# Kernel optimization log

Measured on AMD Instinct MI355X. Metric: run time of the kernel, lower is better.

Reference implementation:

```python
import jax, jax.numpy as jnp
from jax import lax
import numpy as np

HID = 64
NL = 4

def conv2d(x, w, b):
    # x: (N,C,H,W), w: (O,I,kh,kw)
    y = lax.conv_general_dilated(x, w, (1, 1), 'SAME',
                                 dimension_numbers=('NCHW', 'OIHW', 'NCHW'))
    return y + b[None, :, None, None]


def stlstm_cell(x, h, c, m, Wx, bx, Wh, bh, Wm, bm, Wo, bo, Wl, bl):
    # standard PredRNN SpatioTemporalLSTM cell
    xc = conv2d(x, Wx, bx)            # 7*HID channels
    hc = conv2d(h, Wh, bh)            # 4*HID
    mc = conv2d(m, Wm, bm)            # 3*HID
    ix, fx, gx, ixp, fxp, gxp, ox = jnp.split(xc, 7, axis=1)
    ih, fh, gh, oh = jnp.split(hc, 4, axis=1)
    im, fm, gm = jnp.split(mc, 3, axis=1)
    i_t = jax.nn.sigmoid(ix + ih)
    f_t = jax.nn.sigmoid(fx + fh)
    g_t = jnp.tanh(gx + gh)
    c_new = f_t * c + i_t * g_t
    i_tp = jax.nn.sigmoid(ixp + im)
    f_tp = jax.nn.sigmoid(fxp + fm)
    g_tp = jnp.tanh(gxp + gm)
    m_new = f_tp * m + i_tp * g_tp
    mem = jnp.concatenate([c_new, m_new], axis=1)  # 2*HID
    o_t = jax.nn.sigmoid(ox + oh + conv2d(mem, Wo, bo))
    h_new = o_t * jnp.tanh(conv2d(mem, Wl, bl))
    return h_new, c_new, m_new


def setup_inputs() -> dict:
    key = jax.random.key(0)
    ks = jax.random.split(key, 16)
    B, L, C, H, W = 8, 10, 1, 256, 256
    x = jax.random.normal(ks[0], (B, L, C, H, W), dtype=jnp.float32)
    s = 0.02
    d = dict(
        x=x, in_len=10, out_len=10,
        Wx=jax.random.normal(ks[1], (NL, 7 * HID, HID, 3, 3), jnp.float32) * s,
        bx=jnp.zeros((NL, 7 * HID), jnp.float32),
        Wh=jax.random.normal(ks[2], (NL, 4 * HID, HID, 3, 3), jnp.float32) * s,
        bh=jnp.zeros((NL, 4 * HID), jnp.float32),
        Wm=jax.random.normal(ks[3], (NL, 3 * HID, HID, 3, 3), jnp.float32) * s,
        bm=jnp.zeros((NL, 3 * HID), jnp.float32),
        Wo=jax.random.normal(ks[4], (NL, HID, 2 * HID, 3, 3), jnp.float32) * s,
        bo=jnp.zeros((NL, HID), jnp.float32),
        Wl=jax.random.normal(ks[5], (NL, HID, 2 * HID, 1, 1), jnp.float32) * s,
        bl=jnp.zeros((NL, HID), jnp.float32),
        Wd=jax.random.normal(ks[6], (64, HID, 3, 3), jnp.float32) * s,
        bd=jnp.zeros((64,), jnp.float32),
    )
    return d


def reference(x, in_len, out_len, Wx, bx, Wh, bh, Wm, bm, Wo, bo, Wl, bl, Wd, bd):
    B, L, C, H, W = x.shape
    ph, pw = H // 8, W // 8
    # patch_division: space-to-depth 8x8
    xp = x.reshape(B, L, C, 8, ph, 8, pw).transpose(0, 1, 2, 3, 5, 4, 6)
    xp = xp.reshape(B, L, C * 64, ph, pw)
    T = in_len + out_len - 1  # 19 steps
    pad = jnp.zeros((B, T - in_len, C * 64, ph, pw), xp.dtype)
    xs_seq = jnp.moveaxis(jnp.concatenate([xp, pad], axis=1), 1, 0)  # (T,B,64,ph,pw)
    flags = jnp.arange(T) < in_len
    z = jnp.zeros((NL, B, HID, ph, pw), xp.dtype)
    carry0 = (z, z, jnp.zeros((B, HID, ph, pw), xp.dtype),
              jnp.zeros((B, HID, ph, pw), xp.dtype))

    def step(carry, inp):
        hs, cs, m, htop = carry
        xt, flag = inp
        cur = jnp.where(flag, xt, htop)
        new_h, new_c = [], []
        for l in range(NL):
            h, c, m = stlstm_cell(cur, hs[l], cs[l], m,
                                  Wx[l], bx[l], Wh[l], bh[l], Wm[l], bm[l],
                                  Wo[l], bo[l], Wl[l], bl[l])
            new_h.append(h)
            new_c.append(c)
            cur = h
        return (jnp.stack(new_h), jnp.stack(new_c), m, cur), cur

    _, outs = lax.scan(step, carry0, (xs_seq, flags))  # (T,B,HID,ph,pw)
    y = jnp.moveaxis(outs, 0, 1).reshape(B * T, HID, ph, pw)
    y = jax.nn.sigmoid(conv2d(y, Wd, bd)).reshape(B, T, 64, ph, pw)
    # patch_combination: depth-to-space 8x8
    out = y.reshape(B, T, 1, 8, 8, ph, pw).transpose(0, 1, 2, 3, 5, 4, 6)
    out = out.reshape(B, T, 1, 8 * ph, 8 * pw)
    return out
```

## Files before the change

kernel.cpp:

```cpp
#include <hip/hip_runtime.h>
#include <hip/hip_bf16.h>


typedef __bf16 bf16x8 __attribute__((ext_vector_type(8)));
typedef float f32x4 __attribute__((ext_vector_type(4)));

namespace {
constexpr int  T     = 19;
constexpr int  INLEN = 10;

constexpr long OFF_XPB   = 0;
constexpr long OFF_OUTSB = 2621440;
constexpr long OFF_HB    = 7602176;
constexpr long OFF_MB    = 8650752;
constexpr long OFF_C     = 9175040;
constexpr long OFF_M     = 11272192;
constexpr long OFF_MEMB  = 11796480;
constexpr long OFF_OP    = 12320768;
constexpr long OFF_WFA   = 12845056;
constexpr long OFF_WFB   = 13877248;
constexpr long OFF_WFD   = 14041088;
constexpr long OFF_BA    = 14059520;
constexpr long WS_NEEDED_FLOATS = 14061312;
}

__device__ __forceinline__ float sigf(float x)     { return 1.f / (1.f + __expf(-x)); }
__device__ __forceinline__ float tanhfast(float x) { return 2.f / (1.f + __expf(-2.f * x)) - 1.f; }
__device__ __forceinline__ unsigned short f2b(float f) {
  __hip_bfloat16 h = __float2bfloat16(f);
  return __builtin_bit_cast(unsigned short, h);
}
__device__ __forceinline__ f32x4 mfma16(bf16x8 a, bf16x8 b, f32x4 c) {
  return __builtin_amdgcn_mfma_f32_16x16x32_bf16(a, b, c, 0, 0, 0);
}

__global__ __launch_bounds__(448) void kcellA(
    const unsigned short* __restrict__ in0, long in0bs,
    const unsigned short* __restrict__ hB,
    const unsigned short* __restrict__ mBr,
    const unsigned short* __restrict__ wfA,
    const float* __restrict__ bA,
    float* __restrict__ C, float* __restrict__ M,
    unsigned short* __restrict__ mBw,
    unsigned short* __restrict__ memB,
    float* __restrict__ op)
{
  __shared__ __align__(16) char smem[57344];
  unsigned short* sIn = (unsigned short*)smem;
  float* sEx = (float*)smem;

  const int b = blockIdx.x, r0 = blockIdx.y, tid = threadIdx.x;
  const unsigned short* base0 = in0 + (long)b * in0bs;
  const unsigned short* base1 = hB  + (long)b * 65536;
  const unsigned short* base2 = mBr + (long)b * 65536;

  for (int s = tid; s < 3 * 816; s += 448) {
    int inp = s / 816, rem = s - inp * 816;
    int slot = rem >> 3, cg = rem & 7;
    int rr = slot / 34, cl = slot - rr * 34;
    int gr = r0 - 1 + rr, gc = cl - 1;
    const unsigned short* bp = (inp == 0) ? base0 : ((inp == 1) ? base1 : base2);
    uint4 v = make_uint4(0u, 0u, 0u, 0u);
    if ((unsigned)gr < 32u && (unsigned)gc < 32u)
      v = *(const uint4*)(bp + ((long)(gr * 32 + gc) << 6) + cg * 8);
    *(uint4*)(sIn + inp * 6528 + slot * 64 + ((cg ^ (slot & 7)) * 8)) = v;
  }
  __syncthreads();

  const int w = tid >> 6, lane = tid & 63, q = lane >> 4, n16 = lane & 15;
  f32x4 acc[4][2];
  #pragma unroll
  for (int i = 0; i < 4; ++i) { acc[i][0] = (f32x4){0,0,0,0}; acc[i][1] = (f32x4){0,0,0,0}; }

  const unsigned short* sb1 = sIn + ((w < 4) ? 6528 : 13056);
  const unsigned short* wbase = wfA + (long)w * 73728;

  #pragma unroll
  for (int p = 0; p < 2; ++p) {
    const unsigned short* sb = p ? sb1 : sIn;
    #pragma unroll
    for (int tap = 0; tap < 9; ++tap) {
      const int dy = tap / 3, dx = tap - dy * 3;
      #pragma unroll
      for (int cc = 0; cc < 2; ++cc) {
        const unsigned short* wp = wbase + (long)(((p * 9 + tap) * 2 + cc) * 4) * 512 + lane * 8;
        bf16x8 a0 = *(const bf16x8*)(wp);
        bf16x8 a1 = *(const bf16x8*)(wp + 512);
        bf16x8 a2 = *(const bf16x8*)(wp + 1024);
        bf16x8 a3 = *(const bf16x8*)(wp + 1536);
        const int g = cc * 4 + q;
        bf16x8 bf0, bf1;
        { int slot = dy * 34 + n16 + dx;
          bf0 = *(const bf16x8*)(sb + slot * 64 + ((g ^ (slot & 7)) * 8)); }
        { int slot = dy * 34 + 16 + n16 + dx;
          bf1 = *(const bf16x8*)(sb + slot * 64 + ((g ^ (slot & 7)) * 8)); }
        acc[0][0] = mfma16(a0, bf0, acc[0][0]); acc[0][1] = mfma16(a0, bf1, acc[0][1]);
        acc[1][0] = mfma16(a1, bf0, acc[1][0]); acc[1][1] = mfma16(a1, bf1, acc[1][1]);
        acc[2][0] = mfma16(a2, bf0, acc[2][0]); acc[2][1] = mfma16(a2, bf1, acc[2][1]);
        acc[3][0] = mfma16(a3, bf0, acc[3][0]); acc[3][1] = mfma16(a3, bf1, acc[3][1]);
      }
    }
  }

  __syncthreads();
  #pragma unroll
  for (int i = 0; i < 4; ++i)
    #pragma unroll
    for (int j = 0; j < 2; ++j)
      #pragma unroll
      for (int r = 0; r < 4; ++r)
        sEx[w * 2048 + (i * 16 + q * 4 + r) * 32 + (j * 16 + n16)] = acc[i][j][r];
  __syncthreads();

  for (int idx = tid; idx < 2048; idx += 448) {
    const int ch = idx >> 5, pxl = idx & 31;
    const int pxg = r0 * 32 + pxl;
    float iv = sEx[idx]            + bA[ch];
    float fv = sEx[2048 + idx]     + bA[64 + ch];
    float gv = sEx[4096 + idx]     + bA[128 + ch];
    float ov = sEx[6144 + idx]     + bA[192 + ch];
    float i2 = sEx[8192 + idx]     + bA[256 + ch];
    float f2 = sEx[10240 + idx]    + bA[320 + ch];
    float g2 = sEx[12288 + idx]    + bA[384 + ch];
    const long cmo = ((long)b * 64 + ch) * 1024 + pxg;
    float cn = sigf(fv) * C[cmo] + sigf(iv) * tanhfast(gv);
    float mn = sigf(f2) * M[cmo] + sigf(i2) * tanhfast(g2);
    C[cmo] = cn; M[cmo] = mn; op[cmo] = ov;
    const long mo = (long)b * 1024 + pxg;
    memB[mo * 128 + ch]      = f2b(cn);
    memB[mo * 128 + 64 + ch] = f2b(mn);
    mBw[mo * 64 + ch]        = f2b(mn);
  }
}

__global__ __launch_bounds__(512) void kcellB(
    const unsigned short* __restrict__ memB,
    const unsigned short* __restrict__ wfB,
    const float* __restrict__ op, const float* __restrict__ bl,
    unsigned short* __restrict__ hBw, unsigned short* __restrict__ outsBt,
    int writeOuts)
{
  __shared__ __align__(16) char smem[73728];
  unsigned short* sIn = (unsigned short*)smem;
  float* sEx = (float*)smem;

  const int b = blockIdx.x, r0 = blockIdx.y, tid = threadIdx.x;
  const unsigned short* bp = memB + (long)b * 131072;
  for (int s = tid; s < 102 * 16; s += 512) {
    int slot = s >> 4, cg = s & 15;
    int rr = slot / 34, cl = slot - rr * 34;
    int gr = r0 - 1 + rr, gc = cl - 1;
    uint4 v = make_uint4(0u, 0u, 0u, 0u);
    if ((unsigned)gr < 32u && (unsigned)gc < 32u)
      v = *(const uint4*)(bp + ((long)(gr * 32 + gc) << 7) + cg * 8);
    *(uint4*)(sIn + slot * 128 + ((cg ^ (slot & 7)) * 8)) = v;
  }
  __syncthreads();

  const int w = tid >> 6, lane = tid & 63, q = lane >> 4, n16 = lane & 15;
  f32x4 accO[4][2], accL[4][2];
  #pragma unroll
  for (int i = 0; i < 4; ++i) {
    accO[i][0] = (f32x4){0,0,0,0}; accO[i][1] = (f32x4){0,0,0,0};
    accL[i][0] = (f32x4){0,0,0,0}; accL[i][1] = (f32x4){0,0,0,0};
  }

  #pragma unroll
  for (int s5 = 0; s5 < 5; ++s5) {
    const int s = w * 5 + s5;
    const bool isL = (s >= 36);
    const int tap = isL ? 4 : (s >> 2);
    const int cc  = isL ? (s - 36) : (s & 3);
    const int dy = tap / 3, dx = tap - dy * 3;
    const unsigned short* wp = wfB + (long)s * 2048 + lane * 8;
    bf16x8 a0 = *(const bf16x8*)(wp);
    bf16x8 a1 = *(const bf16x8*)(wp + 512);
    bf16x8 a2 = *(const bf16x8*)(wp + 1024);
    bf16x8 a3 = *(const bf16x8*)(wp + 1536);
    const int g = cc * 4 + q;
    bf16x8 bf0, bf1;
    { int slot = dy * 34 + n16 + dx;
      bf0 = *(const bf16x8*)(sIn + slot * 128 + ((g ^ (slot & 7)) * 8)); }
    { int slot = dy * 34 + 16 + n16 + dx;
      bf1 = *(const bf16x8*)(sIn + slot * 128 + ((g ^ (slot & 7)) * 8)); }
    if (isL) {
      accL[0][0] = mfma16(a0, bf0, accL[0][0]); accL[0][1] = mfma16(a0, bf1, accL[0][1]);
      accL[1][0] = mfma16(a1, bf0, accL[1][0]); accL[1][1] = mfma16(a1, bf1, accL[1][1]);
      accL[2][0] = mfma16(a2, bf0, accL[2][0]); accL[2][1] = mfma16(a2, bf1, accL[2][1]);
      accL[3][0] = mfma16(a3, bf0, accL[3][0]); accL[3][1] = mfma16(a3, bf1, accL[3][1]);
    } else {
      accO[0][0] = mfma16(a0, bf0, accO[0][0]); accO[0][1] = mfma16(a0, bf1, accO[0][1]);
      accO[1][0] = mfma16(a1, bf0, accO[1][0]); accO[1][1] = mfma16(a1, bf1, accO[1][1]);
      accO[2][0] = mfma16(a2, bf0, accO[2][0]); accO[2][1] = mfma16(a2, bf1, accO[2][1]);
      accO[3][0] = mfma16(a3, bf0, accO[3][0]); accO[3][1] = mfma16(a3, bf1, accO[3][1]);
    }
  }

  __syncthreads();
  #pragma unroll
  for (int i = 0; i < 4; ++i)
    #pragma unroll
    for (int j = 0; j < 2; ++j)
      #pragma unroll
      for (int r = 0; r < 4; ++r)
        sEx[w * 2048 + (i * 16 + q * 4 + r) * 32 + (j * 16 + n16)] = accO[i][j][r];
  if (w == 7) {
    #pragma unroll
    for (int i = 0; i < 4; ++i)
      #pragma unroll
      for (int j = 0; j < 2; ++j)
        #pragma unroll
        for (int r = 0; r < 4; ++r)
          sEx[16384 + (i * 16 + q * 4 + r) * 32 + (j * 16 + n16)] = accL[i][j][r];
  }
  __syncthreads();

  for (int idx = tid; idx < 2048; idx += 512) {
    const int ch = idx >> 5, pxl = idx & 31;
    const int pxg = r0 * 32 + pxl;
    float o = op[((long)b * 64 + ch) * 1024 + pxg];
    #pragma unroll
    for (int ww = 0; ww < 8; ++ww) o += sEx[ww * 2048 + idx];
    float l = sEx[16384 + idx] + bl[ch];
    unsigned short hv = f2b(sigf(o) * tanhfast(l));
    hBw[((long)b * 1024 + pxg) * 64 + ch] = hv;
    if (writeOuts) outsBt[((long)b * 1024 + pxg) * 64 + ch] = hv;
  }
}

__device__ __forceinline__ void conv3_acc(
    const unsigned short* __restrict__ ip, int ciStride, int ciOff,
    const unsigned short* __restrict__ wf, int ncc, int ccoff,
    unsigned short* sIn, f32x4 (&acc)[4][4])
{
  const int tid = threadIdx.x;
  const int r0  = (int)blockIdx.y * 8;
  for (int s = tid; s < 2720; s += 256) {
    int slot = s >> 3, cg = s & 7;
    int rr = slot / 34, cl = slot - rr * 34;
    int gr = r0 - 1 + rr, gc = cl - 1;
    uint4 v = make_uint4(0u, 0u, 0u, 0u);
    if ((unsigned)gr < 32u && (unsigned)gc < 32u)
      v = *(const uint4*)(ip + (long)(gr * 32 + gc) * ciStride + ciOff + cg * 8);
    *(uint4*)(sIn + slot * 64 + ((cg ^ (slot & 7)) * 8)) = v;
  }
  __syncthreads();
  const int lane = tid & 63, w = tid >> 6;
  const int q = lane >> 4, n16 = lane & 15;
  #pragma unroll
  for (int i = 0; i < 4; ++i)
    #pragma unroll
    for (int j = 0; j < 4; ++j)
      acc[i][j] = (f32x4){0.f, 0.f, 0.f, 0.f};
  #pragma unroll
  for (int tap = 0; tap < 9; ++tap) {
    const int dy = tap / 3, dx = tap - dy * 3;
    #pragma unroll
    for (int cc = 0; cc < 2; ++cc) {
      const unsigned short* wp = wf + (long)(tap * ncc + ccoff + cc) * 2048 + lane * 8;
      bf16x8 a0 = *(const bf16x8*)(wp);
      bf16x8 a1 = *(const bf16x8*)(wp + 512);
      bf16x8 a2 = *(const bf16x8*)(wp + 1024);
      bf16x8 a3 = *(const bf16x8*)(wp + 1536);
      const int cs = cc * 4 + q;
      bf16x8 bfr[4];
      #pragma unroll
      for (int pf = 0; pf < 4; ++pf) {
        int slot = (w * 2 + (pf >> 1) + dy) * 34 + (pf & 1) * 16 + dx + n16;
        bfr[pf] = *(const bf16x8*)(sIn + slot * 64 + ((cs ^ (slot & 7)) * 8));
      }
      #pragma unroll
      for (int j = 0; j < 4; ++j) {
        acc[0][j] = mfma16(a0, bfr[j], acc[0][j]);
        acc[1][j] = mfma16(a1, bfr[j], acc[1][j]);
        acc[2][j] = mfma16(a2, bfr[j], acc[2][j]);
        acc[3][j] = mfma16(a3, bfr[j], acc[3][j]);
      }
    }
  }
}

__global__ __launch_bounds__(256) void kconv_final(
    const unsigned short* __restrict__ outsB,
    const unsigned short* __restrict__ wdf, const float* __restrict__ bd,
    float* __restrict__ dout)
{
  __shared__ __align__(16) unsigned short sIn[21760];
  const int img = blockIdx.x;
  const int b = img / 19, t = img - b * 19;
  f32x4 acc[4][4];
  conv3_acc(outsB + ((long)t * 8 + b) * 65536, 64, 0, wdf, 2, 0, sIn, acc);
  const int tid = threadIdx.x;
  const int lane = tid & 63, w = tid >> 6;
  const int q = lane >> 4, n16 = lane & 15;
  const int r0 = (int)blockIdx.y * 8;
  float* ob = dout + (long)img * 65536;
  #pragma unroll
  for (int i = 0; i < 4; ++i) {
    #pragma unroll
    for (int r = 0; r < 4; ++r) {
      const int co = i * 16 + q * 4 + r;
      const float bv = bd[co];
      #pragma unroll
      for (int j = 0; j < 4; ++j) {
        int row = r0 + w * 2 + (j >> 1);
        int col = (j & 1) * 16 + n16;
        ob[((co >> 3) * 32 + row) * 256 + (co & 7) * 32 + col] = sigf(acc[i][j][r] + bv);
      }
    }
  }
}

__global__ __launch_bounds__(256) void kpatch(const float* __restrict__ x,
                                              unsigned short* __restrict__ xpB)
{
  __shared__ __align__(16) unsigned short sT[2048];
  const int img = blockIdx.x, tid = threadIdx.x;
  const float* xi = x + (long)img * 65536;
  unsigned short* xo = xpB + (long)img * 65536;
  for (int p = 0; p < 32; ++p) {
    __syncthreads();
    int ch = tid >> 2, q0 = (tid & 3) * 8;
    const float* s = xi + ((ch >> 3) * 32 + p) * 256 + (ch & 7) * 32 + q0;
    float4 v0 = *(const float4*)s, v1 = *(const float4*)(s + 4);
    float vv[8] = {v0.x, v0.y, v0.z, v0.w, v1.x, v1.y, v1.z, v1.w};
    #pragma unroll
    for (int k = 0; k < 8; ++k) {
      int qq = q0 + k;
      sT[qq * 64 + (((ch >> 3) ^ (qq & 7)) * 8) + (ch & 7)] = f2b(vv[k]);
    }
    __syncthreads();
    int q = tid >> 3, cg = tid & 7;
    uint4 v = *(const uint4*)(sT + q * 64 + ((cg ^ (q & 7)) * 8));
    *(uint4*)(xo + (long)(p * 32 + q) * 64 + cg * 8) = v;
  }
}

__global__ __launch_bounds__(256) void kprepw(const float* __restrict__ src,
                                              unsigned short* __restrict__ dst,
                                              int Cout, int Cin, int KK)
{
  long n = (long)Cout * Cin * KK;
  long idx = (long)blockIdx.x * 256 + threadIdx.x;
  if (idx >= n) return;
  int ncc = Cin >> 5;
  long tmp = idx >> 3; int e = (int)(idx & 7);
  int lane = (int)(tmp & 63); tmp >>= 6;
  int cf = (int)(tmp & 3); tmp >>= 2;
  int cc = (int)(tmp % ncc); tmp /= ncc;
  int tap = (int)(tmp % KK); int chunk = (int)(tmp / KK);
  int co = chunk * 64 + cf * 16 + (lane & 15);
  int ci = cc * 32 + (lane >> 4) * 8 + e;
  dst[idx] = f2b(src[((long)co * Cin + ci) * KK + tap]);
}

__global__ __launch_bounds__(256) void kpackA(
    const float* __restrict__ Wx, const float* __restrict__ Wh,
    const float* __restrict__ Wm, unsigned short* __restrict__ wfA)
{
  long idx = (long)blockIdx.x * 256 + threadIdx.x;
  if (idx >= 2064384) return;
  int e = (int)(idx & 7);
  long t = idx >> 3;
  int lane = (int)(t & 63); t >>= 6;
  int frag = (int)(t & 3);  t >>= 2;
  int cc   = (int)(t & 1);  t >>= 1;
  int tap  = (int)(t % 9);  t /= 9;
  int p    = (int)(t & 1);  t >>= 1;
  int w    = (int)(t % 7);
  int l    = (int)(t / 7);
  int co = frag * 16 + (lane & 15);
  int ci = cc * 32 + (lane >> 4) * 8 + e;
  const float* src; int row;
  if (w < 4) {
    if (p == 0) { src = Wx + (long)l * 258048; row = (w == 3 ? 384 : w * 64) + co; }
    else        { src = Wh + (long)l * 147456; row = (w == 3 ? 192 : w * 64) + co; }
  } else {
    if (p == 0) { src = Wx + (long)l * 258048; row = 192 + (w - 4) * 64 + co; }
    else        { src = Wm + (long)l * 110592; row = (w - 4) * 64 + co; }
  }
  wfA[idx] = f2b(src[((long)row * 64 + ci) * 9 + tap]);
}

__global__ __launch_bounds__(256) void kpackB(
    const float* __restrict__ Wo, const float* __restrict__ Wl,
    unsigned short* __restrict__ wfB)
{
  long idx = (long)blockIdx.x * 256 + threadIdx.x;
  if (idx >= 327680) return;
  int e = (int)(idx & 7);
  long t = idx >> 3;
  int lane = (int)(t & 63); t >>= 6;
  int frag = (int)(t & 3);  t >>= 2;
  int s    = (int)(t % 40);
  int l    = (int)(t / 40);
  int co = frag * 16 + (lane & 15);
  float v;
  if (s < 36) {
    int tap = s >> 2, cc = s & 3;
    int ci = cc * 32 + (lane >> 4) * 8 + e;
    v = Wo[(long)l * 73728 + ((long)co * 128 + ci) * 9 + tap];
  } else {
    int cc = s - 36;
    int ci = cc * 32 + (lane >> 4) * 8 + e;
    v = Wl[(long)l * 8192 + (long)co * 128 + ci];
  }
  wfB[idx] = f2b(v);
}

__global__ __launch_bounds__(256) void kpackbA(
    const float* __restrict__ bx, const float* __restrict__ bh,
    const float* __restrict__ bm, const float* __restrict__ bo,
    float* __restrict__ bA)
{
  int idx = blockIdx.x * 256 + threadIdx.x;
  if (idx >= 1792) return;
  int ch = idx & 63, w = (idx >> 6) % 7, l = (idx >> 6) / 7;
  const float* bxl = bx + l * 448;
  const float* bhl = bh + l * 256;
  const float* bml = bm + l * 192;
  const float* bol = bo + l * 64;
  float v;
  if (w < 3)       v = bxl[w * 64 + ch] + bhl[w * 64 + ch];
  else if (w == 3) v = bxl[384 + ch] + bhl[192 + ch] + bol[ch];
  else             v = bxl[192 + (w - 4) * 64 + ch] + bml[(w - 4) * 64 + ch];
  bA[idx] = v;
}

extern "C" void kernel_launch(void* const* d_in, const int* in_sizes, int n_in,
                              void* d_out, int out_size, void* d_ws, size_t ws_size,
                              hipStream_t stream)
{
  (void)in_sizes; (void)n_in; (void)out_size;
  if (ws_size < WS_NEEDED_FLOATS * sizeof(float)) return;

  const float* x  = (const float*)d_in[0];
  const float* Wx = (const float*)d_in[3];
  const float* bx = (const float*)d_in[4];
  const float* Wh = (const float*)d_in[5];
  const float* bh = (const float*)d_in[6];
  const float* Wm = (const float*)d_in[7];
  const float* bm = (const float*)d_in[8];
  const float* Wo = (const float*)d_in[9];
  const float* bo = (const float*)d_in[10];
  const float* Wl = (const float*)d_in[11];
  const float* bl = (const float*)d_in[12];
  const float* Wd = (const float*)d_in[13];
  const float* bd = (const float*)d_in[14];
  float* ws  = (float*)d_ws;
  float* out = (float*)d_out;

  unsigned short* xpB   = (unsigned short*)(ws + OFF_XPB);
  unsigned short* outsB = (unsigned short*)(ws + OFF_OUTSB);
  unsigned short* hB    = (unsigned short*)(ws + OFF_HB);
  unsigned short* mB0   = (unsigned short*)(ws + OFF_MB);
  unsigned short* mB1   = mB0 + 524288;
  float*          C     = ws + OFF_C;
  float*          M     = ws + OFF_M;
  unsigned short* memB  = (unsigned short*)(ws + OFF_MEMB);
  float*          OP    = ws + OFF_OP;
  unsigned short* wfA   = (unsigned short*)(ws + OFF_WFA);
  unsigned short* wfB   = (unsigned short*)(ws + OFF_WFB);
  unsigned short* wfD   = (unsigned short*)(ws + OFF_WFD);
  float*          bA    = ws + OFF_BA;

  kpackA<<<dim3(8064), 256, 0, stream>>>(Wx, Wh, Wm, wfA);
  kpackB<<<dim3(1280), 256, 0, stream>>>(Wo, Wl, wfB);
  kpackbA<<<dim3(7), 256, 0, stream>>>(bx, bh, bm, bo, bA);
  kprepw<<<dim3(144), 256, 0, stream>>>(Wd, wfD, 64, 64, 9);
  kpatch<<<dim3(80), 256, 0, stream>>>(x, xpB);
  hipMemsetAsync(ws + OFF_HB, 0, (OFF_MEMB - OFF_HB) * sizeof(float), stream);

  for (int t = 0; t < T; ++t) {
    for (int l = 0; l < 4; ++l) {
      const int cell = t * 4 + l;
      const unsigned short* in0; long ibs;
      if (l == 0) {
        if (t < INLEN) { in0 = xpB + (long)t * 65536; ibs = 655360; }
        else           { in0 = outsB + (long)(t - 1) * 524288; ibs = 65536; }
      } else {
        in0 = hB + (long)(l - 1) * 524288; ibs = 65536;
      }
      const unsigned short* mBr = (cell & 1) ? mB1 : mB0;
      unsigned short*       mBw = (cell & 1) ? mB0 : mB1;
      kcellA<<<dim3(8, 32), 448, 0, stream>>>(
          in0, ibs, hB + (long)l * 524288, mBr,
          wfA + (long)l * 516096, bA + l * 448,
          C + (long)l * 524288, M, mBw, memB, OP);
      kcellB<<<dim3(8, 32), 512, 0, stream>>>(
          memB, wfB + (long)l * 81920, OP, bl + l * 64,
          hB + (long)l * 524288, outsB + (long)t * 524288, (l == 3) ? 1 : 0);
    }
  }
  kconv_final<<<dim3(152, 4), 256, 0, stream>>>(outsB, wfD, bd, out);
}
```

Measured before the change: 2.654 ms.

## Fuse all recurrent cell launches into one persistent kernel with grid barriers

Replaces the 152 separate kcellA/kcellB launches with a single persistent kernel of 256 blocks. The blocks loop over all timesteps and layers and synchronise between phases with an atomic-counter grid barrier. The B phase is also reworked to run on 7 waves instead of 8, with the 1x1 conv given to the last wave. This is meant to remove per-launch overhead and launch gaps. In exchange it depends on all 256 blocks being co-resident, and every cell now pays two spin-wait barriers.

```diff
diff --git a/kernel.cpp b/kernel.cpp
--- a/kernel.cpp
+++ b/kernel.cpp
@@ -21,7 +21,8 @@
 constexpr long OFF_WFB   = 13877248;
 constexpr long OFF_WFD   = 14041088;
 constexpr long OFF_BA    = 14059520;
-constexpr long WS_NEEDED_FLOATS = 14061312;
+constexpr long OFF_BAR   = 14061312;
+constexpr long WS_NEEDED_FLOATS = 14061376;
 }
 
 __device__ __forceinline__ float sigf(float x)     { return 1.f / (1.f + __expf(-x)); }
@@ -34,197 +35,224 @@
   return __builtin_amdgcn_mfma_f32_16x16x32_bf16(a, b, c, 0, 0, 0);
 }
 
-__global__ __launch_bounds__(448) void kcellA(
-    const unsigned short* __restrict__ in0, long in0bs,
-    const unsigned short* __restrict__ hB,
-    const unsigned short* __restrict__ mBr,
-    const unsigned short* __restrict__ wfA,
-    const float* __restrict__ bA,
-    float* __restrict__ C, float* __restrict__ M,
-    unsigned short* __restrict__ mBw,
-    unsigned short* __restrict__ memB,
-    float* __restrict__ op)
+__device__ __forceinline__ void gridbar(unsigned* cnt, unsigned target) {
+  __syncthreads();
+  if (threadIdx.x == 0) {
+    __threadfence();
+    __hip_atomic_fetch_add(cnt, 1u, __ATOMIC_RELAXED, __HIP_MEMORY_SCOPE_AGENT);
+    while (__hip_atomic_load(cnt, __ATOMIC_RELAXED, __HIP_MEMORY_SCOPE_AGENT) < target)
+      __builtin_amdgcn_s_sleep(2);
+    __threadfence();
+  }
+  __syncthreads();
+}
+
+__global__ __launch_bounds__(448, 2) void kcells(
+    const unsigned short* xpB, unsigned short* outsB, unsigned short* hB,
+    unsigned short* mB0, unsigned short* mB1,
+    float* C, float* M, unsigned short* memB, float* op,
+    const unsigned short* wfA, const unsigned short* wfB,
+    const float* bA, const float* blv, unsigned* bar)
 {
   __shared__ __align__(16) char smem[57344];
   unsigned short* sIn = (unsigned short*)smem;
   float* sEx = (float*)smem;
 
-  const int b = blockIdx.x, r0 = blockIdx.y, tid = threadIdx.x;
-  const unsigned short* base0 = in0 + (long)b * in0bs;
-  const unsigned short* base1 = hB  + (long)b * 65536;
-  const unsigned short* base2 = mBr + (long)b * 65536;
-
-  for (int s = tid; s < 3 * 816; s += 448) {
-    int inp = s / 816, rem = s - inp * 816;
-    int slot = rem >> 3, cg = rem & 7;
-    int rr = slot / 34, cl = slot - rr * 34;
-    int gr = r0 - 1 + rr, gc = cl - 1;
-    const unsigned short* bp = (inp == 0) ? base0 : ((inp == 1) ? base1 : base2);
-    uint4 v = make_uint4(0u, 0u, 0u, 0u);
-    if ((unsigned)gr < 32u && (unsigned)gc < 32u)
-      v = *(const uint4*)(bp + ((long)(gr * 32 + gc) << 6) + cg * 8);
-    *(uint4*)(sIn + inp * 6528 + slot * 64 + ((cg ^ (slot & 7)) * 8)) = v;
-  }
-  __syncthreads();
-
+  const int blk = blockIdx.x;
+  const int b = blk >> 5, r0 = blk & 31;
+  const int tid = threadIdx.x;
   const int w = tid >> 6, lane = tid & 63, q = lane >> 4, n16 = lane & 15;
-  f32x4 acc[4][2];
-  #pragma unroll
-  for (int i = 0; i < 4; ++i) { acc[i][0] = (f32x4){0,0,0,0}; acc[i][1] = (f32x4){0,0,0,0}; }
-
-  const unsigned short* sb1 = sIn + ((w < 4) ? 6528 : 13056);
-  const unsigned short* wbase = wfA + (long)w * 73728;
-
-  #pragma unroll
-  for (int p = 0; p < 2; ++p) {
-    const unsigned short* sb = p ? sb1 : sIn;
-    #pragma unroll
-    for (int tap = 0; tap < 9; ++tap) {
-      const int dy = tap / 3, dx = tap - dy * 3;
-      #pragma unroll
-      for (int cc = 0; cc < 2; ++cc) {
-        const unsigned short* wp = wbase + (long)(((p * 9 + tap) * 2 + cc) * 4) * 512 + lane * 8;
-        bf16x8 a0 = *(const bf16x8*)(wp);
-        bf16x8 a1 = *(const bf16x8*)(wp + 512);
-        bf16x8 a2 = *(const bf16x8*)(wp + 1024);
-        bf16x8 a3 = *(const bf16x8*)(wp + 1536);
-        const int g = cc * 4 + q;
-        bf16x8 bf0, bf1;
-        { int slot = dy * 34 + n16 + dx;
-          bf0 = *(const bf16x8*)(sb + slot * 64 + ((g ^ (slot & 7)) * 8)); }
-        { int slot = dy * 34 + 16 + n16 + dx;
-          bf1 = *(const bf16x8*)(sb + slot * 64 + ((g ^ (slot & 7)) * 8)); }
-        acc[0][0] = mfma16(a0, bf0, acc[0][0]); acc[0][1] = mfma16(a0, bf1, acc[0][1]);
-        acc[1][0] = mfma16(a1, bf0, acc[1][0]); acc[1][1] = mfma16(a1, bf1, acc[1][1]);
-        acc[2][0] = mfma16(a2, bf0, acc[2][0]); acc[2][1] = mfma16(a2, bf1, acc[2][1]);
-        acc[3][0] = mfma16(a3, bf0, acc[3][0]); acc[3][1] = mfma16(a3, bf1, acc[3][1]);
-      }
+  unsigned nbar = 0;
+
+  for (int cell = 0; cell < T * 4; ++cell) {
+    const int t = cell >> 2, l = cell & 3;
+    const unsigned short* in0; long ibs;
+    if (l == 0) {
+      if (t < INLEN) { in0 = xpB + (long)t * 65536; ibs = 655360; }
+      else           { in0 = outsB + (long)(t - 1) * 524288; ibs = 65536; }
+    } else {
+      in0 = hB + (long)(l - 1) * 524288; ibs = 65536;
     }
-  }
-
-  __syncthreads();
-  #pragma unroll
-  for (int i = 0; i < 4; ++i)
-    #pragma unroll
-    for (int j = 0; j < 2; ++j)
-      #pragma unroll
-      for (int r = 0; r < 4; ++r)
-        sEx[w * 2048 + (i * 16 + q * 4 + r) * 32 + (j * 16 + n16)] = acc[i][j][r];
-  __syncthreads();
-
-  for (int idx = tid; idx < 2048; idx += 448) {
-    const int ch = idx >> 5, pxl = idx & 31;
-    const int pxg = r0 * 32 + pxl;
-    float iv = sEx[idx]            + bA[ch];
-    float fv = sEx[2048 + idx]     + bA[64 + ch];
-    float gv = sEx[4096 + idx]     + bA[128 + ch];
-    float ov = sEx[6144 + idx]     + bA[192 + ch];
-    float i2 = sEx[8192 + idx]     + bA[256 + ch];
-    float f2 = sEx[10240 + idx]    + bA[320 + ch];
-    float g2 = sEx[12288 + idx]    + bA[384 + ch];
-    const long cmo = ((long)b * 64 + ch) * 1024 + pxg;
-    float cn = sigf(fv) * C[cmo] + sigf(iv) * tanhfast(gv);
-    float mn = sigf(f2) * M[cmo] + sigf(i2) * tanhfast(g2);
-    C[cmo] = cn; M[cmo] = mn; op[cmo] = ov;
-    const long mo = (long)b * 1024 + pxg;
-    memB[mo * 128 + ch]      = f2b(cn);
-    memB[mo * 128 + 64 + ch] = f2b(mn);
-    mBw[mo * 64 + ch]        = f2b(mn);
-  }
-}
-
-__global__ __launch_bounds__(512) void kcellB(
-    const unsigned short* __restrict__ memB,
-    const unsigned short* __restrict__ wfB,
-    const float* __restrict__ op, const float* __restrict__ bl,
-    unsigned short* __restrict__ hBw, unsigned short* __restrict__ outsBt,
-    int writeOuts)
-{
-  __shared__ __align__(16) char smem[73728];
-  unsigned short* sIn = (unsigned short*)smem;
-  float* sEx = (float*)smem;
-
-  const int b = blockIdx.x, r0 = blockIdx.y, tid = threadIdx.x;
-  const unsigned short* bp = memB + (long)b * 131072;
-  for (int s = tid; s < 102 * 16; s += 512) {
-    int slot = s >> 4, cg = s & 15;
-    int rr = slot / 34, cl = slot - rr * 34;
-    int gr = r0 - 1 + rr, gc = cl - 1;
-    uint4 v = make_uint4(0u, 0u, 0u, 0u);
-    if ((unsigned)gr < 32u && (unsigned)gc < 32u)
-      v = *(const uint4*)(bp + ((long)(gr * 32 + gc) << 7) + cg * 8);
-    *(uint4*)(sIn + slot * 128 + ((cg ^ (slot & 7)) * 8)) = v;
-  }
-  __syncthreads();
-
-  const int w = tid >> 6, lane = tid & 63, q = lane >> 4, n16 = lane & 15;
-  f32x4 accO[4][2], accL[4][2];
-  #pragma unroll
-  for (int i = 0; i < 4; ++i) {
-    accO[i][0] = (f32x4){0,0,0,0}; accO[i][1] = (f32x4){0,0,0,0};
-    accL[i][0] = (f32x4){0,0,0,0}; accL[i][1] = (f32x4){0,0,0,0};
-  }
-
-  #pragma unroll
-  for (int s5 = 0; s5 < 5; ++s5) {
-    const int s = w * 5 + s5;
-    const bool isL = (s >= 36);
-    const int tap = isL ? 4 : (s >> 2);
-    const int cc  = isL ? (s - 36) : (s & 3);
-    const int dy = tap / 3, dx = tap - dy * 3;
-    const unsigned short* wp = wfB + (long)s * 2048 + lane * 8;
-    bf16x8 a0 = *(const bf16x8*)(wp);
-    bf16x8 a1 = *(const bf16x8*)(wp + 512);
-    bf16x8 a2 = *(const bf16x8*)(wp + 1024);
-    bf16x8 a3 = *(const bf16x8*)(wp + 1536);
-    const int g = cc * 4 + q;
-    bf16x8 bf0, bf1;
-    { int slot = dy * 34 + n16 + dx;
-      bf0 = *(const bf16x8*)(sIn + slot * 128 + ((g ^ (slot & 7)) * 8)); }
-    { int slot = dy * 34 + 16 + n16 + dx;
-      bf1 = *(const bf16x8*)(sIn + slot * 128 + ((g ^ (slot & 7)) * 8)); }
-    if (isL) {
-      accL[0][0] = mfma16(a0, bf0, accL[0][0]); accL[0][1] = mfma16(a0, bf1, accL[0][1]);
-      accL[1][0] = mfma16(a1, bf0, accL[1][0]); accL[1][1] = mfma16(a1, bf1, accL[1][1]);
-      accL[2][0] = mfma16(a2, bf0, accL[2][0]); accL[2][1] = mfma16(a2, bf1, accL[2][1]);
-      accL[3][0] = mfma16(a3, bf0, accL[3][0]); accL[3][1] = mfma16(a3, bf1, accL[3][1]);
-    } else {
-      accO[0][0] = mfma16(a0, bf0, accO[0][0]); accO[0][1] = mfma16(a0, bf1, accO[0][1]);
-      accO[1][0] = mfma16(a1, bf0, accO[1][0]); accO[1][1] = mfma16(a1, bf1, accO[1][1]);
-      accO[2][0] = mfma16(a2, bf0, accO[2][0]); accO[2][1] = mfma16(a2, bf1, accO[2][1]);
-      accO[3][0] = mfma16(a3, bf0, accO[3][0]); accO[3][1] = mfma16(a3, bf1, accO[3][1]);
+    const unsigned short* mBr = (cell & 1) ? mB1 : mB0;
+    unsigned short*       mBw = (cell & 1) ? mB0 : mB1;
+    const unsigned short* wAl = wfA + (long)l * 516096;
+    const unsigned short* wBl = wfB + (long)l * 81920;
+    const float* bAl = bA + l * 448;
+    float* Cl = C + (long)l * 524288;
+
+    {
+      const unsigned short* base0 = in0 + (long)b * ibs;
+      const unsigned short* base1 = hB + (long)l * 524288 + ((long)b << 16);
+      const unsigned short* base2 = mBr + ((long)b << 16);
+      for (int s = tid; s < 3 * 816; s += 448) {
+        int inp = s / 816, rem = s - inp * 816;
+        int slot = rem >> 3, cg = rem & 7;
+        int rr = slot / 34, cl2 = slot - rr * 34;
+        int gr = r0 - 1 + rr, gc = cl2 - 1;
+        const unsigned short* bp = (inp == 0) ? base0 : ((inp == 1) ? base1 : base2);
+        uint4 v = make_uint4(0u, 0u, 0u, 0u);
+        if ((unsigned)gr < 32u && (unsigned)gc < 32u)
+          v = *(const uint4*)(bp + ((long)(gr * 32 + gc) << 6) + cg * 8);
+        *(uint4*)(sIn + inp * 6528 + slot * 64 + ((cg ^ (slot & 7)) * 8)) = v;
+      }
+      __syncthreads();
+
+      f32x4 acc[4][2];
+      #pragma unroll
+      for (int i = 0; i < 4; ++i) {
+        acc[i][0] = (f32x4){0.f,0.f,0.f,0.f};
+        acc[i][1] = (f32x4){0.f,0.f,0.f,0.f};
+      }
+      const unsigned short* sb1 = sIn + ((w < 4) ? 6528 : 13056);
+      const unsigned short* wbase = wAl + (long)w * 73728;
+
+      #pragma unroll
+      for (int p = 0; p < 2; ++p) {
+        const unsigned short* sb = p ? sb1 : sIn;
+        #pragma unroll
+        for (int tap = 0; tap < 9; ++tap) {
+          const int dy = tap / 3, dx = tap - dy * 3;
+          #pragma unroll
+          for (int cc = 0; cc < 2; ++cc) {
+            const unsigned short* wp = wbase + (long)(((p * 9 + tap) * 2 + cc) * 4) * 512 + lane * 8;
+            bf16x8 a0 = *(const bf16x8*)(wp);
+            bf16x8 a1 = *(const bf16x8*)(wp + 512);
+            bf16x8 a2 = *(const bf16x8*)(wp + 1024);
+            bf16x8 a3 = *(const bf16x8*)(wp + 1536);
+            const int g = cc * 4 + q;
+            bf16x8 bf0, bf1;
+            { int slot = dy * 34 + n16 + dx;
+              bf0 = *(const bf16x8*)(sb + slot * 64 + ((g ^ (slot & 7)) * 8)); }
+            { int slot = dy * 34 + 16 + n16 + dx;
+              bf1 = *(const bf16x8*)(sb + slot * 64 + ((g ^ (slot & 7)) * 8)); }
+            acc[0][0] = mfma16(a0, bf0, acc[0][0]); acc[0][1] = mfma16(a0, bf1, acc[0][1]);
+            acc[1][0] = mfma16(a1, bf0, acc[1][0]); acc[1][1] = mfma16(a1, bf1, acc[1][1]);
+            acc[2][0] = mfma16(a2, bf0, acc[2][0]); acc[2][1] = mfma16(a2, bf1, acc[2][1]);
+            acc[3][0] = mfma16(a3, bf0, acc[3][0]); acc[3][1] = mfma16(a3, bf1, acc[3][1]);
+          }
+        }
+      }
+
+      __syncthreads();
+      #pragma unroll
+      for (int i = 0; i < 4; ++i)
+        #pragma unroll
+        for (int j = 0; j < 2; ++j)
+          #pragma unroll
+          for (int r = 0; r < 4; ++r)
+            sEx[w * 2048 + (i * 16 + q * 4 + r) * 32 + (j * 16 + n16)] = acc[i][j][r];
+      __syncthreads();
+
+      for (int idx = tid; idx < 2048; idx += 448) {
+        const int ch = idx >> 5, pxl = idx & 31;
+        const int pxg = r0 * 32 + pxl;
+        float iv = sEx[idx]         + bAl[ch];
+        float fv = sEx[2048 + idx]  + bAl[64 + ch];
+        float gv = sEx[4096 + idx]  + bAl[128 + ch];
+        float ov = sEx[6144 + idx]  + bAl[192 + ch];
+        float i2 = sEx[8192 + idx]  + bAl[256 + ch];
+        float f2 = sEx[10240 + idx] + bAl[320 + ch];
+        float g2 = sEx[12288 + idx] + bAl[384 + ch];
+        const long cmo = ((long)b * 64 + ch) * 1024 + pxg;
+        float cn = sigf(fv) * Cl[cmo] + sigf(iv) * tanhfast(gv);
+        float mn = sigf(f2) * M[cmo] + sigf(i2) * tanhfast(g2);
+        Cl[cmo] = cn; M[cmo] = mn; op[cmo] = ov;
+        const long mo = (long)b * 1024 + pxg;
+        memB[mo * 128 + ch]      = f2b(cn);
+        memB[mo * 128 + 64 + ch] = f2b(mn);
+        mBw[mo * 64 + ch]        = f2b(mn);
+      }
     }
-  }
-
-  __syncthreads();
-  #pragma unroll
-  for (int i = 0; i < 4; ++i)
-    #pragma unroll
-    for (int j = 0; j < 2; ++j)
-      #pragma unroll
-      for (int r = 0; r < 4; ++r)
-        sEx[w * 2048 + (i * 16 + q * 4 + r) * 32 + (j * 16 + n16)] = accO[i][j][r];
-  if (w == 7) {
-    #pragma unroll
-    for (int i = 0; i < 4; ++i)
-      #pragma unroll
-      for (int j = 0; j < 2; ++j)
+    gridbar(bar, (++nbar) * 256u);
+
+    {
+      const unsigned short* bp = memB + ((long)b << 17);
+      for (int s = tid; s < 1632; s += 448) {
+        int slot = s >> 4, cg = s & 15;
+        int rr = slot / 34, cl2 = slot - rr * 34;
+        int gr = r0 - 1 + rr, gc = cl2 - 1;
+        uint4 v = make_uint4(0u, 0u, 0u, 0u);
+        if ((unsigned)gr < 32u && (unsigned)gc < 32u)
+          v = *(const uint4*)(bp + ((long)(gr * 32 + gc) << 7) + cg * 8);
+        *(uint4*)(sIn + slot * 128 + ((cg ^ (slot & 7)) * 8)) = v;
+      }
+      __syncthreads();
+
+      f32x4 accA[4][2];
+      #pragma unroll
+      for (int f = 0; f < 4; ++f) {
+        accA[f][0] = (f32x4){0.f,0.f,0.f,0.f};
+        accA[f][1] = (f32x4){0.f,0.f,0.f,0.f};
+      }
+      if (w < 6) {
         #pragma unroll
-        for (int r = 0; r < 4; ++r)
-          sEx[16384 + (i * 16 + q * 4 + r) * 32 + (j * 16 + n16)] = accL[i][j][r];
-  }
-  __syncthreads();
-
-  for (int idx = tid; idx < 2048; idx += 512) {
-    const int ch = idx >> 5, pxl = idx & 31;
-    const int pxg = r0 * 32 + pxl;
-    float o = op[((long)b * 64 + ch) * 1024 + pxg];
-    #pragma unroll
-    for (int ww = 0; ww < 8; ++ww) o += sEx[ww * 2048 + idx];
-    float l = sEx[16384 + idx] + bl[ch];
-    unsigned short hv = f2b(sigf(o) * tanhfast(l));
-    hBw[((long)b * 1024 + pxg) * 64 + ch] = hv;
-    if (writeOuts) outsBt[((long)b * 1024 + pxg) * 64 + ch] = hv;
+        for (int k5 = 0; k5 < 6; ++k5) {
+          const int s = w * 6 + k5;
+          const int tap = s >> 2, cc = s & 3;
+          const int dy = tap / 3, dx = tap - dy * 3;
+          const unsigned short* wp = wBl + (long)s * 2048 + lane * 8;
+          bf16x8 a0 = *(const bf16x8*)(wp);
+          bf16x8 a1 = *(const bf16x8*)(wp + 512);
+          bf16x8 a2 = *(const bf16x8*)(wp + 1024);
+          bf16x8 a3 = *(const bf16x8*)(wp + 1536);
+          const int g = cc * 4 + q;
+          bf16x8 bf0, bf1;
+          { int slot = dy * 34 + n16 + dx;
+            bf0 = *(const bf16x8*)(sIn + slot * 128 + ((g ^ (slot & 7)) * 8)); }
+          { int slot = dy * 34 + 16 + n16 + dx;
+            bf1 = *(const bf16x8*)(sIn + slot * 128 + ((g ^ (slot & 7)) * 8)); }
+          accA[0][0] = mfma16(a0, bf0, accA[0][0]); accA[0][1] = mfma16(a0, bf1, accA[0][1]);
+          accA[1][0] = mfma16(a1, bf0, accA[1][0]); accA[1][1] = mfma16(a1, bf1, accA[1][1]);
+          accA[2][0] = mfma16(a2, bf0, accA[2][0]); accA[2][1] = mfma16(a2, bf1, accA[2][1]);
+          accA[3][0] = mfma16(a3, bf0, accA[3][0]); accA[3][1] = mfma16(a3, bf1, accA[3][1]);
+        }
+      } else {
+        #pragma unroll
+        for (int cc = 0; cc < 4; ++cc) {
+          const int s = 36 + cc;
+          const unsigned short* wp = wBl + (long)s * 2048 + lane * 8;
+          bf16x8 a0 = *(const bf16x8*)(wp);
+          bf16x8 a1 = *(const bf16x8*)(wp + 512);
+          bf16x8 a2 = *(const bf16x8*)(wp + 1024);
+          bf16x8 a3 = *(const bf16x8*)(wp + 1536);
+          const int g = cc * 4 + q;
+          bf16x8 bf0, bf1;
+          { int slot = 34 + n16 + 1;
+            bf0 = *(const bf16x8*)(sIn + slot * 128 + ((g ^ (slot & 7)) * 8)); }
+          { int slot = 34 + 16 + n16 + 1;
+            bf1 = *(const bf16x8*)(sIn + slot * 128 + ((g ^ (slot & 7)) * 8)); }
+          accA[0][0] = mfma16(a0, bf0, accA[0][0]); accA[0][1] = mfma16(a0, bf1, accA[0][1]);
+          accA[1][0] = mfma16(a1, bf0, accA[1][0]); accA[1][1] = mfma16(a1, bf1, accA[1][1]);
+          accA[2][0] = mfma16(a2, bf0, accA[2][0]); accA[2][1] = mfma16(a2, bf1, accA[2][1]);
+          accA[3][0] = mfma16(a3, bf0, accA[3][0]); accA[3][1] = mfma16(a3, bf1, accA[3][1]);
+        }
+      }
+      __syncthreads();
+      #pragma unroll
+      for (int i = 0; i < 4; ++i)
+        #pragma unroll
+        for (int j = 0; j < 2; ++j)
+          #pragma unroll
+          for (int r = 0; r < 4; ++r)
+            sEx[w * 2048 + (i * 16 + q * 4 + r) * 32 + (j * 16 + n16)] = accA[i][j][r];
+      __syncthreads();
+
+      unsigned short* hRow = hB + (long)l * 524288;
+      unsigned short* oRow = outsB + (long)t * 524288;
+      const int writeOuts = (l == 3);
+      for (int idx = tid; idx < 2048; idx += 448) {
+        const int ch = idx >> 5, pxl = idx & 31;
+        const int pxg = r0 * 32 + pxl;
+        float o = op[((long)b * 64 + ch) * 1024 + pxg];
+        #pragma unroll
+        for (int ww = 0; ww < 6; ++ww) o += sEx[ww * 2048 + idx];
+        float lg = sEx[12288 + idx] + blv[l * 64 + ch];
+        unsigned short hv = f2b(sigf(o) * tanhfast(lg));
+        hRow[((long)b * 1024 + pxg) * 64 + ch] = hv;
+        if (writeOuts) oRow[((long)b * 1024 + pxg) * 64 + ch] = hv;
+      }
+    }
+    gridbar(bar, (++nbar) * 256u);
   }
 }
 
@@ -463,6 +491,7 @@
   unsigned short* wfB   = (unsigned short*)(ws + OFF_WFB);
   unsigned short* wfD   = (unsigned short*)(ws + OFF_WFD);
   float*          bA    = ws + OFF_BA;
+  unsigned*       bar   = (unsigned*)(ws + OFF_BAR);
 
   kpackA<<<dim3(8064), 256, 0, stream>>>(Wx, Wh, Wm, wfA);
   kpackB<<<dim3(1280), 256, 0, stream>>>(Wo, Wl, wfB);
@@ -470,27 +499,11 @@
   kprepw<<<dim3(144), 256, 0, stream>>>(Wd, wfD, 64, 64, 9);
   kpatch<<<dim3(80), 256, 0, stream>>>(x, xpB);
   hipMemsetAsync(ws + OFF_HB, 0, (OFF_MEMB - OFF_HB) * sizeof(float), stream);
-
-  for (int t = 0; t < T; ++t) {
-    for (int l = 0; l < 4; ++l) {
-      const int cell = t * 4 + l;
-      const unsigned short* in0; long ibs;
-      if (l == 0) {
-        if (t < INLEN) { in0 = xpB + (long)t * 65536; ibs = 655360; }
-        else           { in0 = outsB + (long)(t - 1) * 524288; ibs = 65536; }
-      } else {
-        in0 = hB + (long)(l - 1) * 524288; ibs = 65536;
-      }
-      const unsigned short* mBr = (cell & 1) ? mB1 : mB0;
-      unsigned short*       mBw = (cell & 1) ? mB0 : mB1;
-      kcellA<<<dim3(8, 32), 448, 0, stream>>>(
-          in0, ibs, hB + (long)l * 524288, mBr,
-          wfA + (long)l * 516096, bA + l * 448,
-          C + (long)l * 524288, M, mBw, memB, OP);
-      kcellB<<<dim3(8, 32), 512, 0, stream>>>(
-          memB, wfB + (long)l * 81920, OP, bl + l * 64,
-          hB + (long)l * 524288, outsB + (long)t * 524288, (l == 3) ? 1 : 0);
-    }
-  }
+  hipMemsetAsync(bar, 0, 64, stream);
+
+  kcells<<<dim3(256), 448, 0, stream>>>(
+      xpB, outsB, hB, mB0, mB1, C, M, memB, OP,
+      wfA, wfB, bA, bl, bar);
+
   kconv_final<<<dim3(152, 4), 256, 0, stream>>>(outsB, wfD, bd, out);
 }
```

Result: slower. 6.240 ms (+135.1%).

## Split cellA by C/M gate groups and tile two rows per block

Applied to the files above, without the earlier changes.

kcellA now launches a z dimension that separates the C-path gates (i,f,g,o from x and h) from the M-path gates (i',f',g' from x and m). Each block stages only two input tensors and covers two output rows, so every weight fragment feeds four B tiles instead of two. The output gate is written straight from registers to op, skipping the shared-memory exchange. The trade-off is that the x input is staged and convolved in both z halves, one warp idles in z=1 blocks, and register pressure rises with 16 accumulators per warp.

```diff
diff --git a/kernel.cpp b/kernel.cpp
--- a/kernel.cpp
+++ b/kernel.cpp
@@ -34,108 +34,137 @@
   return __builtin_amdgcn_mfma_f32_16x16x32_bf16(a, b, c, 0, 0, 0);
 }
 
-__global__ __launch_bounds__(448) void kcellA(
+__global__ __launch_bounds__(256) void kcellA(
     const unsigned short* __restrict__ in0, long in0bs,
-    const unsigned short* __restrict__ hB,
+    const unsigned short* __restrict__ hBl,
     const unsigned short* __restrict__ mBr,
-    const unsigned short* __restrict__ wfA,
-    const float* __restrict__ bA,
-    float* __restrict__ C, float* __restrict__ M,
+    const unsigned short* __restrict__ wfAl,
+    const float* __restrict__ bAl,
+    float* __restrict__ Cl, float* __restrict__ M,
     unsigned short* __restrict__ mBw,
     unsigned short* __restrict__ memB,
     float* __restrict__ op)
 {
-  __shared__ __align__(16) char smem[57344];
+  __shared__ __align__(16) char smem[49152];
   unsigned short* sIn = (unsigned short*)smem;
   float* sEx = (float*)smem;
 
-  const int b = blockIdx.x, r0 = blockIdx.y, tid = threadIdx.x;
+  const int b = blockIdx.x, rp = blockIdx.y, z = blockIdx.z, tid = threadIdx.x;
+  const int r0 = rp * 2;
+
   const unsigned short* base0 = in0 + (long)b * in0bs;
-  const unsigned short* base1 = hB  + (long)b * 65536;
-  const unsigned short* base2 = mBr + (long)b * 65536;
-
-  for (int s = tid; s < 3 * 816; s += 448) {
-    int inp = s / 816, rem = s - inp * 816;
-    int slot = rem >> 3, cg = rem & 7;
-    int rr = slot / 34, cl = slot - rr * 34;
-    int gr = r0 - 1 + rr, gc = cl - 1;
-    const unsigned short* bp = (inp == 0) ? base0 : ((inp == 1) ? base1 : base2);
+  const unsigned short* base1 = z ? (mBr + ((long)b << 16)) : (hBl + ((long)b << 16));
+
+  for (int s = tid; s < 2176; s += 256) {
+    const int inp = (s >= 1088);
+    const int rem = s - inp * 1088;
+    const int slot = rem >> 3, cg = rem & 7;
+    const int rr = slot / 34, cl = slot - rr * 34;
+    const int gr = r0 - 1 + rr, gc = cl - 1;
+    const unsigned short* bp = inp ? base1 : base0;
     uint4 v = make_uint4(0u, 0u, 0u, 0u);
     if ((unsigned)gr < 32u && (unsigned)gc < 32u)
       v = *(const uint4*)(bp + ((long)(gr * 32 + gc) << 6) + cg * 8);
-    *(uint4*)(sIn + inp * 6528 + slot * 64 + ((cg ^ (slot & 7)) * 8)) = v;
+    *(uint4*)(sIn + inp * 8704 + slot * 64 + ((cg ^ (slot & 7)) * 8)) = v;
   }
   __syncthreads();
 
   const int w = tid >> 6, lane = tid & 63, q = lane >> 4, n16 = lane & 15;
-  f32x4 acc[4][2];
-  #pragma unroll
-  for (int i = 0; i < 4; ++i) { acc[i][0] = (f32x4){0,0,0,0}; acc[i][1] = (f32x4){0,0,0,0}; }
-
-  const unsigned short* sb1 = sIn + ((w < 4) ? 6528 : 13056);
-  const unsigned short* wbase = wfA + (long)w * 73728;
-
-  #pragma unroll
-  for (int p = 0; p < 2; ++p) {
-    const unsigned short* sb = p ? sb1 : sIn;
-    #pragma unroll
-    for (int tap = 0; tap < 9; ++tap) {
-      const int dy = tap / 3, dx = tap - dy * 3;
-      #pragma unroll
-      for (int cc = 0; cc < 2; ++cc) {
-        const unsigned short* wp = wbase + (long)(((p * 9 + tap) * 2 + cc) * 4) * 512 + lane * 8;
-        bf16x8 a0 = *(const bf16x8*)(wp);
-        bf16x8 a1 = *(const bf16x8*)(wp + 512);
-        bf16x8 a2 = *(const bf16x8*)(wp + 1024);
-        bf16x8 a3 = *(const bf16x8*)(wp + 1536);
-        const int g = cc * 4 + q;
-        bf16x8 bf0, bf1;
-        { int slot = dy * 34 + n16 + dx;
-          bf0 = *(const bf16x8*)(sb + slot * 64 + ((g ^ (slot & 7)) * 8)); }
-        { int slot = dy * 34 + 16 + n16 + dx;
-          bf1 = *(const bf16x8*)(sb + slot * 64 + ((g ^ (slot & 7)) * 8)); }
-        acc[0][0] = mfma16(a0, bf0, acc[0][0]); acc[0][1] = mfma16(a0, bf1, acc[0][1]);
-        acc[1][0] = mfma16(a1, bf0, acc[1][0]); acc[1][1] = mfma16(a1, bf1, acc[1][1]);
-        acc[2][0] = mfma16(a2, bf0, acc[2][0]); acc[2][1] = mfma16(a2, bf1, acc[2][1]);
-        acc[3][0] = mfma16(a3, bf0, acc[3][0]); acc[3][1] = mfma16(a3, bf1, acc[3][1]);
+  const bool working = z ? (w < 3) : (w < 4);
+  const int gate = z ? (4 + w) : w;
+
+  f32x4 acc[4][4];
+  #pragma unroll
+  for (int i = 0; i < 4; ++i)
+    #pragma unroll
+    for (int pf = 0; pf < 4; ++pf) acc[i][pf] = (f32x4){0.f, 0.f, 0.f, 0.f};
+
+  if (working) {
+    const unsigned short* wbase = wfAl + (long)gate * 73728;
+    #pragma unroll
+    for (int p = 0; p < 2; ++p) {
+      const unsigned short* sb = sIn + p * 8704;
+      #pragma unroll
+      for (int tap = 0; tap < 9; ++tap) {
+        const int dy = tap / 3, dx = tap - dy * 3;
+        #pragma unroll
+        for (int cc = 0; cc < 2; ++cc) {
+          const unsigned short* wp =
+              wbase + (long)(((p * 9 + tap) * 2 + cc) * 4) * 512 + lane * 8;
+          bf16x8 a0 = *(const bf16x8*)(wp);
+          bf16x8 a1 = *(const bf16x8*)(wp + 512);
+          bf16x8 a2 = *(const bf16x8*)(wp + 1024);
+          bf16x8 a3 = *(const bf16x8*)(wp + 1536);
+          const int cs = cc * 4 + q;
+          bf16x8 B[4];
+          #pragma unroll
+          for (int pf = 0; pf < 4; ++pf) {
+            const int slot = ((pf >> 1) + dy) * 34 + (pf & 1) * 16 + dx + n16;
+            B[pf] = *(const bf16x8*)(sb + slot * 64 + ((cs ^ (slot & 7)) * 8));
+          }
+          #pragma unroll
+          for (int pf = 0; pf < 4; ++pf) {
+            acc[0][pf] = mfma16(a0, B[pf], acc[0][pf]);
+            acc[1][pf] = mfma16(a1, B[pf], acc[1][pf]);
+            acc[2][pf] = mfma16(a2, B[pf], acc[2][pf]);
+            acc[3][pf] = mfma16(a3, B[pf], acc[3][pf]);
+          }
+        }
       }
     }
   }
-
-  __syncthreads();
-  #pragma unroll
-  for (int i = 0; i < 4; ++i)
-    #pragma unroll
-    for (int j = 0; j < 2; ++j)
-      #pragma unroll
-      for (int r = 0; r < 4; ++r)
-        sEx[w * 2048 + (i * 16 + q * 4 + r) * 32 + (j * 16 + n16)] = acc[i][j][r];
-  __syncthreads();
-
-  for (int idx = tid; idx < 2048; idx += 448) {
-    const int ch = idx >> 5, pxl = idx & 31;
-    const int pxg = r0 * 32 + pxl;
-    float iv = sEx[idx]            + bA[ch];
-    float fv = sEx[2048 + idx]     + bA[64 + ch];
-    float gv = sEx[4096 + idx]     + bA[128 + ch];
-    float ov = sEx[6144 + idx]     + bA[192 + ch];
-    float i2 = sEx[8192 + idx]     + bA[256 + ch];
-    float f2 = sEx[10240 + idx]    + bA[320 + ch];
-    float g2 = sEx[12288 + idx]    + bA[384 + ch];
+  __syncthreads();
+
+  if (z == 0 && w == 3) {
+    #pragma unroll
+    for (int i = 0; i < 4; ++i)
+      #pragma unroll
+      for (int r = 0; r < 4; ++r) {
+        const int co = i * 16 + q * 4 + r;
+        const float bv = bAl[192 + co];
+        #pragma unroll
+        for (int pf = 0; pf < 4; ++pf) {
+          const int pxg = (r0 + (pf >> 1)) * 32 + (pf & 1) * 16 + n16;
+          op[((long)b * 64 + co) * 1024 + pxg] = acc[i][pf][r] + bv;
+        }
+      }
+  } else if (working) {
+    float* slab = sEx + w * 4096;
+    #pragma unroll
+    for (int i = 0; i < 4; ++i)
+      #pragma unroll
+      for (int r = 0; r < 4; ++r) {
+        const int co = i * 16 + q * 4 + r;
+        #pragma unroll
+        for (int pf = 0; pf < 4; ++pf) {
+          const int pxl = (pf >> 1) * 32 + (pf & 1) * 16 + n16;
+          slab[co * 64 + pxl] = acc[i][pf][r];
+        }
+      }
+  }
+  __syncthreads();
+
+  const int bo0 = z ? 256 : 0;
+  float* state = z ? M : Cl;
+  for (int idx = tid; idx < 4096; idx += 256) {
+    const int ch = idx >> 6, pxl = idx & 63;
+    const int pxg = (r0 + (pxl >> 5)) * 32 + (pxl & 31);
+    const float iv = sEx[idx]           + bAl[bo0 + ch];
+    const float fv = sEx[4096 + idx]    + bAl[bo0 + 64 + ch];
+    const float gv = sEx[8192 + idx]    + bAl[bo0 + 128 + ch];
     const long cmo = ((long)b * 64 + ch) * 1024 + pxg;
-    float cn = sigf(fv) * C[cmo] + sigf(iv) * tanhfast(gv);
-    float mn = sigf(f2) * M[cmo] + sigf(i2) * tanhfast(g2);
-    C[cmo] = cn; M[cmo] = mn; op[cmo] = ov;
+    const float vn = sigf(fv) * state[cmo] + sigf(iv) * tanhfast(gv);
+    state[cmo] = vn;
     const long mo = (long)b * 1024 + pxg;
-    memB[mo * 128 + ch]      = f2b(cn);
-    memB[mo * 128 + 64 + ch] = f2b(mn);
-    mBw[mo * 64 + ch]        = f2b(mn);
+    const unsigned short vb = f2b(vn);
+    memB[mo * 128 + (z ? 64 : 0) + ch] = vb;
+    if (z) mBw[mo * 64 + ch] = vb;
   }
 }
 
 __global__ __launch_bounds__(512) void kcellB(
     const unsigned short* __restrict__ memB,
-    const unsigned short* __restrict__ wfB,
+    const unsigned short* __restrict__ wfBl,
     const float* __restrict__ op, const float* __restrict__ bl,
     unsigned short* __restrict__ hBw, unsigned short* __restrict__ outsBt,
     int writeOuts)
@@ -145,7 +174,7 @@
   float* sEx = (float*)smem;
 
   const int b = blockIdx.x, r0 = blockIdx.y, tid = threadIdx.x;
-  const unsigned short* bp = memB + (long)b * 131072;
+  const unsigned short* bp = memB + ((long)b << 17);
   for (int s = tid; s < 102 * 16; s += 512) {
     int slot = s >> 4, cg = s & 15;
     int rr = slot / 34, cl = slot - rr * 34;
@@ -160,9 +189,9 @@
   const int w = tid >> 6, lane = tid & 63, q = lane >> 4, n16 = lane & 15;
   f32x4 accO[4][2], accL[4][2];
   #pragma unroll
-  for (int i = 0; i < 4; ++i) {
-    accO[i][0] = (f32x4){0,0,0,0}; accO[i][1] = (f32x4){0,0,0,0};
-    accL[i][0] = (f32x4){0,0,0,0}; accL[i][1] = (f32x4){0,0,0,0};
+  for (int f = 0; f < 4; ++f) {
+    accO[f][0] = (f32x4){0.f,0.f,0.f,0.f}; accO[f][1] = (f32x4){0.f,0.f,0.f,0.f};
+    accL[f][0] = (f32x4){0.f,0.f,0.f,0.f}; accL[f][1] = (f32x4){0.f,0.f,0.f,0.f};
   }
 
   #pragma unroll
@@ -172,7 +201,7 @@
     const int tap = isL ? 4 : (s >> 2);
     const int cc  = isL ? (s - 36) : (s & 3);
     const int dy = tap / 3, dx = tap - dy * 3;
-    const unsigned short* wp = wfB + (long)s * 2048 + lane * 8;
+    const unsigned short* wp = wfBl + (long)s * 2048 + lane * 8;
     bf16x8 a0 = *(const bf16x8*)(wp);
     bf16x8 a1 = *(const bf16x8*)(wp + 512);
     bf16x8 a2 = *(const bf16x8*)(wp + 1024);
@@ -483,7 +512,7 @@
       }
       const unsigned short* mBr = (cell & 1) ? mB1 : mB0;
       unsigned short*       mBw = (cell & 1) ? mB0 : mB1;
-      kcellA<<<dim3(8, 32), 448, 0, stream>>>(
+      kcellA<<<dim3(8, 16, 2), 256, 0, stream>>>(
           in0, ibs, hB + (long)l * 524288, mBr,
           wfA + (long)l * 516096, bA + l * 448,
           C + (long)l * 524288, M, mBw, memB, OP);
```

After: 2.743 ms. 3.4% more time.
